# Optimization experiments

Hardware: AMD Instinct MI355X
Metric: run time of the kernel (lower is better)

## Reference

```python
import jax, jax.numpy as jnp
import numpy as np
from jax import lax

DIST_THRESH = 180.0
ATT_THRESH = 0.05


def setup_inputs() -> dict:
    key = jax.random.key(0)
    ks = jax.random.split(key, 6)
    B, N, H, W = 16, 512, 25, 25
    F, Fh = H * W, int(H * W * 1.5)  # 625, 937
    x4 = jax.random.normal(ks[0], (B, N, H, W), dtype=jnp.float32) * 0.25
    attention = jax.random.uniform(ks[1], (B, N, 1, 1), dtype=jnp.float32)
    W1 = jax.random.normal(ks[2], (2, F, Fh), dtype=jnp.float32) * (1.0 / np.sqrt(F))
    b1 = jnp.zeros((Fh,), dtype=jnp.float32)
    W2 = jax.random.normal(ks[3], (2, Fh, F), dtype=jnp.float32) * (1.0 / np.sqrt(Fh))
    b2 = jnp.zeros((F,), dtype=jnp.float32)
    return {"x4": x4, "attention": attention, "W1": W1, "b1": b1, "W2": W2, "b2": b2}


def _build_adjacency(X, att):
    """X: [B,N,F] node features, att: [B,N]. Returns thresholded adjacency [B,N,N]."""
    B, N, F = X.shape
    # pairwise L1 distances, row-by-row scan to avoid materializing [B,N,N,F]
    Xs = jnp.swapaxes(X, 0, 1)  # [N,B,F]

    def row(_, xi):  # xi: [B,F]
        d = jnp.sum(jnp.abs(xi[:, None, :] - X), axis=-1)  # [B,N]
        return None, d

    _, D = lax.scan(row, None, Xs)          # [N,B,N]
    D = jnp.swapaxes(D, 0, 1)               # [B,N,N]
    att_d = jnp.abs(att[:, :, None] - att[:, None, :])  # [B,N,N]
    A = ((D <= DIST_THRESH) & (att_d <= ATT_THRESH)).astype(jnp.float32)
    # original only fills i<j and j<i, diagonal stays 0
    A = A * (1.0 - jnp.eye(N, dtype=jnp.float32))
    return A


def _process_graph(A):
    """A + I, then row-normalize by inverse degree (D^-1 (A+I))."""
    N = A.shape[1]
    A = A + jnp.eye(N, dtype=A.dtype)
    deg = jnp.sum(A, axis=-1)               # [B,N]
    dinv = jnp.where(deg > 0, 1.0 / deg, 0.0)
    return dinv[:, :, None] * A


def _cheb_conv(x, L, Wk, b):
    """ChebConv with K=2 over dense normalized graph L: T0=x, T1=Lx."""
    t1 = jnp.einsum('bij,bjf->bif', L, x)
    return jnp.einsum('bnf,fo->bno', x, Wk[0]) + jnp.einsum('bnf,fo->bno', t1, Wk[1]) + b


def reference(x4, attention, W1, b1, W2, b2):
    B, N, H, W = x4.shape
    X = x4.reshape(B, N, H * W)             # [B,N,625] flow_x
    att = attention[:, :, 0, 0]             # [B,N]
    A = _build_adjacency(X, att)
    L = _process_graph(A)
    h = jax.nn.relu(_cheb_conv(X, L, W1, b1))   # [B,N,937]
    out = jax.nn.relu(_cheb_conv(h, L, W2, b2))  # [B,N,625]
    return out
```

## Files before the change

kernel.cpp:

```cpp
#include <hip/hip_runtime.h>
#include <stdint.h>

typedef uint16_t u16;
typedef uint32_t u32;
typedef __attribute__((ext_vector_type(4))) float f32x4;
typedef __attribute__((ext_vector_type(4))) unsigned short us4;

#define NB   16
#define NN   512
#define FF   625
#define FH   937
#define ROWS 8192
#define KS1  1280
#define KS2  1920
#define NPX  640
#define NPH  960
#define F4   160
#define ITILE 4

using frag_ab = __attribute__((ext_vector_type(8))) short;
using frag_cd = __attribute__((ext_vector_type(4))) float;

__device__ __forceinline__ u16 f32_bf16(float f) {
  union { float f; uint32_t u; } x; x.f = f;
  uint32_t r = x.u + 0x7fffu + ((x.u >> 16) & 1u);
  return (u16)(r >> 16);
}
__device__ __forceinline__ void gload_lds16(const void* g, void* l) {
  __builtin_amdgcn_global_load_lds((__attribute__((address_space(1))) void*)g,
                                   (__attribute__((address_space(3))) void*)l,
                                   16, 0, 0);
}

__global__ __launch_bounds__(256) void prep(
    const float* __restrict__ x4, const float* __restrict__ att,
    const float* __restrict__ W1, const float* __restrict__ W2,
    f32x4* __restrict__ Xpad, u16* __restrict__ Xcat, u16* __restrict__ Xt,
    u16* __restrict__ W1t, u16* __restrict__ W2t,
    float* __restrict__ att_s, u16* __restrict__ ord_g, u32* __restrict__ gmask)
{
  const int blk = blockIdx.x;
  const int tid = threadIdx.x;
  if (blk < 5120) {
    __shared__ float tile[32][33];
    const int xcd = blk & 7, sub = blk >> 3;
    const int b = xcd * 2 + sub / 320;
    const int t = sub % 320;
    const int ft = t % 20, kt = t / 20;
    const int tx = tid & 31, ty = tid >> 5;
    #pragma unroll
    for (int r = 0; r < 4; ++r) {
      const int node = kt * 32 + ty + r * 8;
      const int f = ft * 32 + tx;
      tile[ty + r * 8][tx] = (f < FF) ? x4[((size_t)b * NN + node) * FF + f] : 0.f;
    }
    __syncthreads();
    #pragma unroll
    for (int r = 0; r < 4; ++r) {
      const int f = ft * 32 + ty + r * 8;
      const int node = kt * 32 + tx;
      Xt[((size_t)b * NPX + f) * 512 + node] = f32_bf16(tile[tx][ty + r * 8]);
    }
    const int nd = tid >> 3, sl = tid & 7;
    const int row = b * NN + kt * 32 + nd;
    f32x4 v; us4 o;
    #pragma unroll
    for (int t2 = 0; t2 < 4; ++t2) {
      const float x = tile[nd][sl * 4 + t2];
      v[t2] = x; o[t2] = f32_bf16(x);
    }
    Xpad[(size_t)row * F4 + ft * 8 + sl] = v;
    *(us4*)(Xcat + (size_t)row * KS1 + ft * 32 + sl * 4) = o;
  } else if (blk < 6400) {
    __shared__ float tile[32][33];
    const int bb = blk - 5120;
    const int kt = bb % 40, nt = bb / 40;
    const int tx = tid & 31, ty = tid >> 5;
    #pragma unroll
    for (int r = 0; r < 4; ++r) {
      int k = kt * 32 + ty + r * 8;
      int n = nt * 32 + tx;
      float v = 0.f;
      int c = -1, kk = 0;
      if (k < 625) { c = 0; kk = k; }
      else if (k >= 640 && k < 1265) { c = 1; kk = k - 640; }
      if (c >= 0 && n < FH) v = W1[((size_t)c * 625 + kk) * FH + n];
      tile[ty + r * 8][tx] = v;
    }
    __syncthreads();
    #pragma unroll
    for (int r = 0; r < 4; ++r) {
      int n = nt * 32 + ty + r * 8;
      int k = kt * 32 + tx;
      W1t[(size_t)n * KS1 + k] = f32_bf16(tile[tx][ty + r * 8]);
    }
  } else if (blk < 7600) {
    __shared__ float tile[32][33];
    const int bb = blk - 6400;
    const int kt = bb % 60, nt = bb / 60;
    const int tx = tid & 31, ty = tid >> 5;
    #pragma unroll
    for (int r = 0; r < 4; ++r) {
      int k = kt * 32 + ty + r * 8;
      int n = nt * 32 + tx;
      float v = 0.f;
      int c = -1, kk = 0;
      if (k < 937) { c = 0; kk = k; }
      else if (k >= 960 && k < 1897) { c = 1; kk = k - 960; }
      if (c >= 0 && n < FF) v = W2[((size_t)c * 937 + kk) * FF + n];
      tile[ty + r * 8][tx] = v;
    }
    __syncthreads();
    #pragma unroll
    for (int r = 0; r < 4; ++r) {
      int n = nt * 32 + ty + r * 8;
      int k = kt * 32 + tx;
      W2t[(size_t)n * KS2 + k] = f32_bf16(tile[tx][ty + r * 8]);
    }
  } else {
    __shared__ float sa[512];
    __shared__ u16 so[512];
    const int b = blk - 7600;
    u32* gm = gmask + (size_t)b * 512 * 16;
    for (int s = tid; s < 512 * 16; s += 256) gm[s] = 0;
    sa[tid] = att[b * NN + tid]; sa[tid + 256] = att[b * NN + tid + 256];
    so[tid] = (u16)tid; so[tid + 256] = (u16)(tid + 256);
    for (int k = 2; k <= 512; k <<= 1) {
      for (int j = k >> 1; j > 0; j >>= 1) {
        __syncthreads();
        const int i = ((tid & ~(j - 1)) << 1) | (tid & (j - 1));
        const int p = i | j;
        const bool up = ((i & k) == 0);
        const float va = sa[i], vp = sa[p];
        if ((va > vp) == up) {
          sa[i] = vp; sa[p] = va;
          const u16 t = so[i]; so[i] = so[p]; so[p] = t;
        }
      }
    }
    __syncthreads();
    att_s[b * NN + tid] = sa[tid]; att_s[b * NN + tid + 256] = sa[tid + 256];
    ord_g[b * NN + tid] = so[tid]; ord_g[b * NN + tid + 256] = so[tid + 256];
  }
}

__global__ __launch_bounds__(256) void build_L3(
    const f32x4* __restrict__ Xpad,
    const float* __restrict__ att_s, const u16* __restrict__ ord_g,
    u32* __restrict__ gmask)
{
  __shared__ f32x4 Xi[ITILE][F4];
  __shared__ float as_[512];
  __shared__ u16 ord[512];
  __shared__ int jhi_s;

  const int tid = threadIdx.x;
  const int blk = blockIdx.x;
  const int xcd = blk & 7, sub = blk >> 3;
  const int b = xcd * 2 + (sub >> 7);
  const int s0 = (sub & 127) * ITILE;
  const f32x4* Xb4 = Xpad + (size_t)b * NN * F4;

  as_[tid] = att_s[b * NN + tid]; as_[tid + 256] = att_s[b * NN + tid + 256];
  ord[tid] = ord_g[b * NN + tid]; ord[tid + 256] = ord_g[b * NN + tid + 256];
  __syncthreads();

  for (int s = tid; s < ITILE * F4; s += 256) {
    const int ii = s / F4, k4 = s - ii * F4;
    Xi[ii][k4] = Xb4[(size_t)ord[s0 + ii] * F4 + k4];
  }
  if (tid == 0) {
    const float hit = as_[s0 + ITILE - 1] + 0.05f;
    int lo = 0, hi = 512;
    while (lo < hi) { int m = (lo + hi) >> 1; if (as_[m] <= hit) lo = m + 1; else hi = m; }
    jhi_s = lo;
  }
  __syncthreads();

  const int lane = tid & 63;
  const int wave = tid >> 6;
  const int jhi = jhi_s;
  const f32x4 zero = {0.f, 0.f, 0.f, 0.f};

  for (int sj = s0 + 1 + wave; sj < jhi; sj += 4) {
    const int oj = __builtin_amdgcn_readfirstlane((int)ord[sj]);
    const f32x4* Xj = Xb4 + (size_t)oj * F4;
    const f32x4 xj0 = Xj[lane];
    const f32x4 xj1 = Xj[64 + lane];
    const f32x4 xj2 = (lane < 32) ? Xj[128 + lane] : zero;
    const float aj = as_[sj];
    f32x4 pv;
    #pragma unroll
    for (int ii = 0; ii < ITILE; ++ii) {
      const f32x4 d0 = Xi[ii][lane] - xj0;
      const f32x4 d1 = Xi[ii][64 + lane] - xj1;
      const f32x4 d2 = (lane < 32) ? (Xi[ii][128 + lane] - xj2) : zero;
      float p = 0.f;
      #pragma unroll
      for (int t = 0; t < 4; ++t)
        p += fabsf(d0[t]) + fabsf(d1[t]) + fabsf(d2[t]);
      pv[ii] = p;
    }
    #pragma unroll
    for (int off = 32; off; off >>= 1) {
      f32x4 o;
      o[0] = __shfl_xor(pv[0], off, 64);
      o[1] = __shfl_xor(pv[1], off, 64);
      o[2] = __shfl_xor(pv[2], off, 64);
      o[3] = __shfl_xor(pv[3], off, 64);
      pv += o;
    }
    if (lane == 0) {
      #pragma unroll
      for (int ii = 0; ii < ITILE; ++ii) {
        const int si = s0 + ii;
        if (sj > si && fabsf(aj - as_[si]) <= 0.05f && pv[ii] <= 180.0f) {
          atomicOr(&gmask[((size_t)b * 512 + si) * 16 + (sj >> 5)], 1u << (sj & 31));
          atomicOr(&gmask[((size_t)b * 512 + sj) * 16 + (si >> 5)], 1u << (si & 31));
        }
      }
    }
  }
}

__global__ __launch_bounds__(256) void write_L(
    const u32* __restrict__ gmask, const u16* __restrict__ ord_g,
    u16* __restrict__ L)
{
  __shared__ u32 msk[16][16];
  __shared__ u16 ord[512];
  __shared__ u16 inv[512];
  __shared__ u16 dvs[16];

  const int tid = threadIdx.x;
  const int blk = blockIdx.x;
  const int xcd = blk & 7, sub = blk >> 3;
  const int b = xcd * 2 + (sub >> 5);
  const int s0 = (sub & 31) * 16;

  const u16 o0 = ord_g[b * NN + tid], o1 = ord_g[b * NN + tid + 256];
  ord[tid] = o0; ord[tid + 256] = o1;
  inv[o0] = (u16)tid; inv[o1] = (u16)(tid + 256);
  if (tid < 256) msk[tid >> 4][tid & 15] =
      gmask[((size_t)b * 512 + s0 + (tid >> 4)) * 16 + (tid & 15)];
  __syncthreads();

  if (tid < 16) {
    int d = 0;
    #pragma unroll
    for (int w = 0; w < 16; ++w) d += __popc(msk[tid][w]);
    dvs[tid] = f32_bf16(1.0f / (float)(d + 1));
  }
  __syncthreads();

  #pragma unroll 4
  for (int ii = 0; ii < 16; ++ii) {
    const int oi = ord[s0 + ii];
    const u16 dv = dvs[ii];
    const int j0 = 2 * tid;
    const int sA = inv[j0], sB = inv[j0 + 1];
    const u32 fA = (j0 == oi)     | ((msk[ii][sA >> 5] >> (sA & 31)) & 1u);
    const u32 fB = (j0 + 1 == oi) | ((msk[ii][sB >> 5] >> (sB & 31)) & 1u);
    *(u32*)(L + ((size_t)b * 512 + oi) * 512 + j0) =
        (fA ? (u32)dv : 0u) | ((fB ? (u32)dv : 0u) << 16);
  }
}

template <int KS, int NTILE, int NREAL, int NSTORE, bool RELU, bool BIAS, bool OUT_BF16>
__device__ __forceinline__ void gemm_core(
    const u16* __restrict__ At, const u16* __restrict__ Btt,
    const float* __restrict__ bias, void* __restrict__ C,
    long crow0, int col0, int ldc)
{
  constexpr int NI = NTILE / 32;
  constexpr int BR = NTILE / 32;
  __shared__ __align__(16) u16 Ash[128 * 64];
  __shared__ __align__(16) u16 Bsh[NTILE * 64];

  const int tid  = threadIdx.x;
  const int lane = tid & 63;
  const int wave = tid >> 6;
  const int wm = wave & 1, wn = wave >> 1;
  const int q = lane >> 4, l16 = lane & 15;

  const u16* pa[4]; const u16* pb[BR];
  #pragma unroll
  for (int r = 0; r < 4; ++r) {
    const int ci = r * 256 + tid;
    const int row = ci >> 3, cpos = ci & 7;
    pa[r] = At + (size_t)row * KS + (cpos ^ (row & 7)) * 8;
  }
  #pragma unroll
  for (int r = 0; r < BR; ++r) {
    const int ci = r * 256 + tid;
    const int row = ci >> 3, cpos = ci & 7;
    pb[r] = Btt + (size_t)row * KS + (cpos ^ (row & 7)) * 8;
  }
  const int wbase = (tid & 192) * 8;

  const frag_ab* fA[4][2]; const frag_ab* fB[NI][2];
  #pragma unroll
  for (int mi = 0; mi < 4; ++mi) {
    const int row = wm * 64 + mi * 16 + l16;
    fA[mi][0] = (const frag_ab*)&Ash[row * 64 + ((q    ) ^ (l16 & 7)) * 8];
    fA[mi][1] = (const frag_ab*)&Ash[row * 64 + ((q + 4) ^ (l16 & 7)) * 8];
  }
  #pragma unroll
  for (int ni = 0; ni < NI; ++ni) {
    const int row = wn * (NTILE / 2) + ni * 16 + l16;
    fB[ni][0] = (const frag_ab*)&Bsh[row * 64 + ((q    ) ^ (l16 & 7)) * 8];
    fB[ni][1] = (const frag_ab*)&Bsh[row * 64 + ((q + 4) ^ (l16 & 7)) * 8];
  }

  frag_cd acc[4][NI] = {};

  constexpr int KT = KS / 64;
  for (int kt = 0; kt < KT; ++kt) {
    __syncthreads();
    #pragma unroll
    for (int r = 0; r < 4; ++r) { gload_lds16(pa[r], &Ash[r * 2048 + wbase]); pa[r] += 64; }
    #pragma unroll
    for (int r = 0; r < BR; ++r) { gload_lds16(pb[r], &Bsh[r * 2048 + wbase]); pb[r] += 64; }
    __syncthreads();

    #pragma unroll
    for (int kk = 0; kk < 2; ++kk) {
      frag_ab av[4], bv[NI];
      #pragma unroll
      for (int mi = 0; mi < 4; ++mi) av[mi] = *fA[mi][kk];
      #pragma unroll
      for (int ni = 0; ni < NI; ++ni) bv[ni] = *fB[ni][kk];
      #pragma unroll
      for (int mi = 0; mi < 4; ++mi)
        #pragma unroll
        for (int ni = 0; ni < NI; ++ni)
          acc[mi][ni] = __builtin_amdgcn_mfma_f32_16x16x32_bf16(
              av[mi], bv[ni], acc[mi][ni], 0, 0, 0);
    }
  }

  #pragma unroll
  for (int ni = 0; ni < NI; ++ni) {
    const int col = col0 + wn * (NTILE / 2) + ni * 16 + l16;
    if (col >= NSTORE) continue;
    const bool ok = (col < NREAL);
    float bvv = 0.f;
    if (BIAS) bvv = ok ? bias[col] : 0.f;
    #pragma unroll
    for (int mi = 0; mi < 4; ++mi) {
      #pragma unroll
      for (int r = 0; r < 4; ++r) {
        const long rowg = crow0 + wm * 64 + mi * 16 + q * 4 + r;
        float v = acc[mi][ni][r];
        if (BIAS) v += bvv;
        if (RELU) v = fmaxf(v, 0.f);
        if (!ok) v = 0.f;
        if (OUT_BF16) ((u16*)C)[rowg * (size_t)ldc + col] = f32_bf16(v);
        else          ((float*)C)[rowg * (size_t)ldc + col] = v;
      }
    }
  }
}

template <int KS, int NTILE, int NREAL, int NSTORE, bool RELU, bool BIAS, bool OUT_BF16>
__global__ __launch_bounds__(256) void gemm_dense(
    const u16* __restrict__ A, const u16* __restrict__ Bt,
    const float* __restrict__ bias, void* __restrict__ C, int ldc)
{
  const int x = blockIdx.x;
  const int mt = ((x & 7) << 3) | (x >> 3);
  gemm_core<KS, NTILE, NREAL, NSTORE, RELU, BIAS, OUT_BF16>(
      A + (size_t)mt * 128 * KS, Bt + (size_t)blockIdx.y * NTILE * KS,
      bias, C, (long)mt * 128, blockIdx.y * NTILE, ldc);
}

template <int NP>
__global__ __launch_bounds__(256) void spmm(
    const u16* __restrict__ L, const u16* __restrict__ Bt,
    u16* __restrict__ C, int ldc)
{
  constexpr int TPB = 4 * (NP / 64);
  const int blk = blockIdx.x;
  const int xcd = blk & 7, sub = blk >> 3;
  const int b = xcd * 2 + sub / TPB;
  const int t = sub % TPB;
  const int mt = t & 3, nt = t >> 2;
  gemm_core<512, 64, NP, NP, false, false, true>(
      L + ((size_t)b * 512 + mt * 128) * 512,
      Bt + ((size_t)b * NP + nt * 64) * 512,
      nullptr, C, (long)b * 512 + mt * 128, nt * 64, ldc);
}

__global__ __launch_bounds__(256) void transpose_h(
    const u16* __restrict__ hcat, u16* __restrict__ ht)
{
  __shared__ u16 tile[32][34];
  const int blk = blockIdx.x;
  const int xcd = blk & 7, sub = blk >> 3;
  const int b = xcd * 2 + sub / 480;
  const int t = sub % 480;
  const int kt = t % 16, nt = t / 16;
  const int tid = threadIdx.x;
  const int tx = tid & 31, ty = tid >> 5;
  #pragma unroll
  for (int r = 0; r < 4; ++r) {
    const int node = kt * 32 + ty + r * 8;
    const int n = nt * 32 + tx;
    tile[ty + r * 8][tx] = hcat[((size_t)b * NN + node) * KS2 + n];
  }
  __syncthreads();
  #pragma unroll
  for (int r = 0; r < 4; ++r) {
    const int n = nt * 32 + ty + r * 8;
    const int node = kt * 32 + tx;
    ht[((size_t)b * NPH + n) * 512 + node] = tile[tx][ty + r * 8];
  }
}

extern "C" void kernel_launch(void* const* d_in, const int* in_sizes, int n_in,
                              void* d_out, int out_size, void* d_ws, size_t ws_size,
                              hipStream_t stream) {
  const float* x4  = (const float*)d_in[0];
  const float* att = (const float*)d_in[1];
  const float* W1  = (const float*)d_in[2];
  const float* b1  = (const float*)d_in[3];
  const float* W2  = (const float*)d_in[4];
  const float* b2  = (const float*)d_in[5];
  float* out = (float*)d_out;

  char* ws = (char*)d_ws;
  f32x4* Xpad = (f32x4*)ws;
  u16* ht = (u16*)ws;       ws += (size_t)ROWS * F4 * 16;
  u16* Xcat = (u16*)ws;  ws += (size_t)ROWS * KS1 * 2;
  u16* hcat = (u16*)ws;  ws += (size_t)ROWS * KS2 * 2;
  u16* W1t  = (u16*)ws;  ws += (size_t)1024 * KS1 * 2;
  u16* W2t  = (u16*)ws;  ws += (size_t)640 * KS2 * 2;
  u16* Lm   = (u16*)ws;  ws += (size_t)NB * 512 * 512 * 2;
  u16* Xt   = (u16*)ws;  ws += (size_t)NB * NPX * 512 * 2;
  u32* gmask = (u32*)ws; ws += (size_t)ROWS * 16 * 4;
  float* att_s = (float*)ws; ws += (size_t)NB * NN * 4;
  u16* ord_g   = (u16*)ws;   ws += (size_t)NB * NN * 2;

  prep<<<dim3(7616), 256, 0, stream>>>(x4, att, W1, W2, Xpad, Xcat, Xt,
                                       W1t, W2t, att_s, ord_g, gmask);
  build_L3<<<dim3(2048), 256, 0, stream>>>(Xpad, att_s, ord_g, gmask);
  write_L<<<dim3(512), 256, 0, stream>>>(gmask, ord_g, Lm);
  spmm<NPX><<<dim3(640), 256, 0, stream>>>(Lm, Xt, Xcat + NPX, KS1);
  gemm_dense<KS1, 128, FH, NPH, true, true, true>
      <<<dim3(64, 8), 256, 0, stream>>>(Xcat, W1t, b1, (void*)hcat, KS2);
  transpose_h<<<dim3(7680), 256, 0, stream>>>(hcat, ht);
  spmm<NPH><<<dim3(960), 256, 0, stream>>>(Lm, ht, hcat + NPH, KS2);
  gemm_dense<KS2, 64, FF, FF, true, true, false>
      <<<dim3(64, 10), 256, 0, stream>>>(hcat, W2t, b2, (void*)out, FF);
}
```

Baseline: 222.9 us.

## Halve GEMM M-tile to 64, hold Xi rows in registers, use DPP reductions

The shared GEMM core gains an MTILE parameter, and both the spmm and dense GEMM launches drop from 128-row to 64-row tiles. This doubles the block count so more of the device's compute units are busy and waves hide latency better, at the cost of less reuse of B per block. In the pairwise-distance kernel, the query rows are loaded from LDS into registers once instead of on every j iteration. The last four steps of the wave reduction now use DPP row shifts instead of shuffles. The register caching raises register pressure, and the smaller tiles mean more global and LDS traffic per FLOP.

```diff
diff --git a/kernel.cpp b/kernel.cpp
--- a/kernel.cpp
+++ b/kernel.cpp
@@ -30,6 +30,13 @@
   __builtin_amdgcn_global_load_lds((__attribute__((address_space(1))) void*)g,
                                    (__attribute__((address_space(3))) void*)l,
                                    16, 0, 0);
+}
+template <int CTRL>
+__device__ __forceinline__ float dpp_addf(float x) {
+  union { float f; int i; } a, b;
+  a.f = x;
+  b.i = __builtin_amdgcn_update_dpp(0, a.i, CTRL, 0xF, 0xF, true);
+  return x + b.f;
 }
 
 __global__ __launch_bounds__(256) void prep(
@@ -144,7 +151,7 @@
   }
 }
 
-__global__ __launch_bounds__(256) void build_L3(
+__global__ __launch_bounds__(256) void build_L4(
     const f32x4* __restrict__ Xpad,
     const float* __restrict__ att_s, const u16* __restrict__ ord_g,
     u32* __restrict__ gmask)
@@ -181,6 +188,14 @@
   const int wave = tid >> 6;
   const int jhi = jhi_s;
   const f32x4 zero = {0.f, 0.f, 0.f, 0.f};
+
+  f32x4 a0[ITILE], a1[ITILE], a2[ITILE];
+  #pragma unroll
+  for (int ii = 0; ii < ITILE; ++ii) {
+    a0[ii] = Xi[ii][lane];
+    a1[ii] = Xi[ii][64 + lane];
+    a2[ii] = (lane < 32) ? Xi[ii][128 + lane] : zero;
+  }
 
   for (int sj = s0 + 1 + wave; sj < jhi; sj += 4) {
     const int oj = __builtin_amdgcn_readfirstlane((int)ord[sj]);
@@ -192,9 +207,9 @@
     f32x4 pv;
     #pragma unroll
     for (int ii = 0; ii < ITILE; ++ii) {
-      const f32x4 d0 = Xi[ii][lane] - xj0;
-      const f32x4 d1 = Xi[ii][64 + lane] - xj1;
-      const f32x4 d2 = (lane < 32) ? (Xi[ii][128 + lane] - xj2) : zero;
+      const f32x4 d0 = a0[ii] - xj0;
+      const f32x4 d1 = a1[ii] - xj1;
+      const f32x4 d2 = a2[ii] - xj2;
       float p = 0.f;
       #pragma unroll
       for (int t = 0; t < 4; ++t)
@@ -202,14 +217,17 @@
       pv[ii] = p;
     }
     #pragma unroll
-    for (int off = 32; off; off >>= 1) {
-      f32x4 o;
-      o[0] = __shfl_xor(pv[0], off, 64);
-      o[1] = __shfl_xor(pv[1], off, 64);
-      o[2] = __shfl_xor(pv[2], off, 64);
-      o[3] = __shfl_xor(pv[3], off, 64);
-      pv += o;
-    }
+    for (int t = 0; t < 4; ++t) pv[t] += __shfl_xor(pv[t], 32, 64);
+    #pragma unroll
+    for (int t = 0; t < 4; ++t) pv[t] += __shfl_xor(pv[t], 16, 64);
+    #pragma unroll
+    for (int t = 0; t < 4; ++t) pv[t] = dpp_addf<0x128>(pv[t]);
+    #pragma unroll
+    for (int t = 0; t < 4; ++t) pv[t] = dpp_addf<0x124>(pv[t]);
+    #pragma unroll
+    for (int t = 0; t < 4; ++t) pv[t] = dpp_addf<0x122>(pv[t]);
+    #pragma unroll
+    for (int t = 0; t < 4; ++t) pv[t] = dpp_addf<0x121>(pv[t]);
     if (lane == 0) {
       #pragma unroll
       for (int ii = 0; ii < ITILE; ++ii) {
@@ -266,15 +284,18 @@
   }
 }
 
-template <int KS, int NTILE, int NREAL, int NSTORE, bool RELU, bool BIAS, bool OUT_BF16>
+template <int KS, int MTILE, int NTILE, int NREAL, int NSTORE,
+          bool RELU, bool BIAS, bool OUT_BF16>
 __device__ __forceinline__ void gemm_core(
     const u16* __restrict__ At, const u16* __restrict__ Btt,
     const float* __restrict__ bias, void* __restrict__ C,
     long crow0, int col0, int ldc)
 {
+  constexpr int MI = MTILE / 32;
   constexpr int NI = NTILE / 32;
+  constexpr int AR = MTILE / 32;
   constexpr int BR = NTILE / 32;
-  __shared__ __align__(16) u16 Ash[128 * 64];
+  __shared__ __align__(16) u16 Ash[MTILE * 64];
   __shared__ __align__(16) u16 Bsh[NTILE * 64];
 
   const int tid  = threadIdx.x;
@@ -283,9 +304,9 @@
   const int wm = wave & 1, wn = wave >> 1;
   const int q = lane >> 4, l16 = lane & 15;
 
-  const u16* pa[4]; const u16* pb[BR];
-  #pragma unroll
-  for (int r = 0; r < 4; ++r) {
+  const u16* pa[AR]; const u16* pb[BR];
+  #pragma unroll
+  for (int r = 0; r < AR; ++r) {
     const int ci = r * 256 + tid;
     const int row = ci >> 3, cpos = ci & 7;
     pa[r] = At + (size_t)row * KS + (cpos ^ (row & 7)) * 8;
@@ -298,10 +319,10 @@
   }
   const int wbase = (tid & 192) * 8;
 
-  const frag_ab* fA[4][2]; const frag_ab* fB[NI][2];
-  #pragma unroll
-  for (int mi = 0; mi < 4; ++mi) {
-    const int row = wm * 64 + mi * 16 + l16;
+  const frag_ab* fA[MI][2]; const frag_ab* fB[NI][2];
+  #pragma unroll
+  for (int mi = 0; mi < MI; ++mi) {
+    const int row = wm * (MTILE / 2) + mi * 16 + l16;
     fA[mi][0] = (const frag_ab*)&Ash[row * 64 + ((q    ) ^ (l16 & 7)) * 8];
     fA[mi][1] = (const frag_ab*)&Ash[row * 64 + ((q + 4) ^ (l16 & 7)) * 8];
   }
@@ -312,26 +333,26 @@
     fB[ni][1] = (const frag_ab*)&Bsh[row * 64 + ((q + 4) ^ (l16 & 7)) * 8];
   }
 
-  frag_cd acc[4][NI] = {};
+  frag_cd acc[MI][NI] = {};
 
   constexpr int KT = KS / 64;
   for (int kt = 0; kt < KT; ++kt) {
     __syncthreads();
     #pragma unroll
-    for (int r = 0; r < 4; ++r) { gload_lds16(pa[r], &Ash[r * 2048 + wbase]); pa[r] += 64; }
+    for (int r = 0; r < AR; ++r) { gload_lds16(pa[r], &Ash[r * 2048 + wbase]); pa[r] += 64; }
     #pragma unroll
     for (int r = 0; r < BR; ++r) { gload_lds16(pb[r], &Bsh[r * 2048 + wbase]); pb[r] += 64; }
     __syncthreads();
 
     #pragma unroll
     for (int kk = 0; kk < 2; ++kk) {
-      frag_ab av[4], bv[NI];
-      #pragma unroll
-      for (int mi = 0; mi < 4; ++mi) av[mi] = *fA[mi][kk];
+      frag_ab av[MI], bv[NI];
+      #pragma unroll
+      for (int mi = 0; mi < MI; ++mi) av[mi] = *fA[mi][kk];
       #pragma unroll
       for (int ni = 0; ni < NI; ++ni) bv[ni] = *fB[ni][kk];
       #pragma unroll
-      for (int mi = 0; mi < 4; ++mi)
+      for (int mi = 0; mi < MI; ++mi)
         #pragma unroll
         for (int ni = 0; ni < NI; ++ni)
           acc[mi][ni] = __builtin_amdgcn_mfma_f32_16x16x32_bf16(
@@ -347,10 +368,10 @@
     float bvv = 0.f;
     if (BIAS) bvv = ok ? bias[col] : 0.f;
     #pragma unroll
-    for (int mi = 0; mi < 4; ++mi) {
+    for (int mi = 0; mi < MI; ++mi) {
       #pragma unroll
       for (int r = 0; r < 4; ++r) {
-        const long rowg = crow0 + wm * 64 + mi * 16 + q * 4 + r;
+        const long rowg = crow0 + wm * (MTILE / 2) + mi * 16 + q * 4 + r;
         float v = acc[mi][ni][r];
         if (BIAS) v += bvv;
         if (RELU) v = fmaxf(v, 0.f);
@@ -362,16 +383,18 @@
   }
 }
 
-template <int KS, int NTILE, int NREAL, int NSTORE, bool RELU, bool BIAS, bool OUT_BF16>
+template <int KS, int MTILE, int NTILE, int NREAL, int NSTORE,
+          bool RELU, bool BIAS, bool OUT_BF16>
 __global__ __launch_bounds__(256) void gemm_dense(
     const u16* __restrict__ A, const u16* __restrict__ Bt,
     const float* __restrict__ bias, void* __restrict__ C, int ldc)
 {
+  constexpr int MTPX = (ROWS / MTILE) / 8;
   const int x = blockIdx.x;
-  const int mt = ((x & 7) << 3) | (x >> 3);
-  gemm_core<KS, NTILE, NREAL, NSTORE, RELU, BIAS, OUT_BF16>(
-      A + (size_t)mt * 128 * KS, Bt + (size_t)blockIdx.y * NTILE * KS,
-      bias, C, (long)mt * 128, blockIdx.y * NTILE, ldc);
+  const int mt = (x & 7) * MTPX + (x >> 3);
+  gemm_core<KS, MTILE, NTILE, NREAL, NSTORE, RELU, BIAS, OUT_BF16>(
+      A + (size_t)mt * MTILE * KS, Bt + (size_t)blockIdx.y * NTILE * KS,
+      bias, C, (long)mt * MTILE, blockIdx.y * NTILE, ldc);
 }
 
 template <int NP>
@@ -379,16 +402,16 @@
     const u16* __restrict__ L, const u16* __restrict__ Bt,
     u16* __restrict__ C, int ldc)
 {
-  constexpr int TPB = 4 * (NP / 64);
+  constexpr int TPB = 8 * (NP / 64);
   const int blk = blockIdx.x;
   const int xcd = blk & 7, sub = blk >> 3;
   const int b = xcd * 2 + sub / TPB;
   const int t = sub % TPB;
-  const int mt = t & 3, nt = t >> 2;
-  gemm_core<512, 64, NP, NP, false, false, true>(
-      L + ((size_t)b * 512 + mt * 128) * 512,
+  const int mt = t & 7, nt = t >> 3;
+  gemm_core<512, 64, 64, NP, NP, false, false, true>(
+      L + ((size_t)b * 512 + mt * 64) * 512,
       Bt + ((size_t)b * NP + nt * 64) * 512,
-      nullptr, C, (long)b * 512 + mt * 128, nt * 64, ldc);
+      nullptr, C, (long)b * 512 + mt * 64, nt * 64, ldc);
 }
 
 __global__ __launch_bounds__(256) void transpose_h(
@@ -443,13 +466,13 @@
 
   prep<<<dim3(7616), 256, 0, stream>>>(x4, att, W1, W2, Xpad, Xcat, Xt,
                                        W1t, W2t, att_s, ord_g, gmask);
-  build_L3<<<dim3(2048), 256, 0, stream>>>(Xpad, att_s, ord_g, gmask);
+  build_L4<<<dim3(2048), 256, 0, stream>>>(Xpad, att_s, ord_g, gmask);
   write_L<<<dim3(512), 256, 0, stream>>>(gmask, ord_g, Lm);
-  spmm<NPX><<<dim3(640), 256, 0, stream>>>(Lm, Xt, Xcat + NPX, KS1);
-  gemm_dense<KS1, 128, FH, NPH, true, true, true>
-      <<<dim3(64, 8), 256, 0, stream>>>(Xcat, W1t, b1, (void*)hcat, KS2);
+  spmm<NPX><<<dim3(1280), 256, 0, stream>>>(Lm, Xt, Xcat + NPX, KS1);
+  gemm_dense<KS1, 64, 128, FH, NPH, true, true, true>
+      <<<dim3(128, 8), 256, 0, stream>>>(Xcat, W1t, b1, (void*)hcat, KS2);
   transpose_h<<<dim3(7680), 256, 0, stream>>>(hcat, ht);
-  spmm<NPH><<<dim3(960), 256, 0, stream>>>(Lm, ht, hcat + NPH, KS2);
-  gemm_dense<KS2, 64, FF, FF, true, true, false>
-      <<<dim3(64, 10), 256, 0, stream>>>(hcat, W2t, b2, (void*)out, FF);
-}
+  spmm<NPH><<<dim3(1920), 256, 0, stream>>>(Lm, ht, hcat + NPH, KS2);
+  gemm_dense<KS2, 64, 64, FF, FF, true, true, false>
+      <<<dim3(128, 10), 256, 0, stream>>>(hcat, W2t, b2, (void*)out, FF);
+}
```

Result: no change. 225.0 us (+0.9%).
